# Optimization experiments

Measured on AMD Instinct MI355X. Metric: run time of the kernel, lower is better.

## Reference

```python
import jax, jax.numpy as jnp
import numpy as np

N = 100000
E = 3200000
D = 256
H = 8
DH = D // H
COEF = 1.0 / (DH ** 0.5)


def setup_inputs() -> dict:
    key = jax.random.key(0)
    ks = jax.random.split(key, 7)
    x = jax.random.normal(ks[0], (N, D), dtype=jnp.float32)
    W_qkv = jax.random.normal(ks[1], (D, 3 * D), dtype=jnp.float32) * (D ** -0.5)
    b_qkv = jax.random.normal(ks[2], (3 * D,), dtype=jnp.float32) * 0.01
    W_out = jax.random.normal(ks[3], (2 * D, D), dtype=jnp.float32) * ((2 * D) ** -0.5)
    b_out = jax.random.normal(ks[4], (D,), dtype=jnp.float32) * 0.01
    src = jax.random.randint(ks[5], (E,), 0, N, dtype=jnp.int64)
    dst = jax.random.randint(ks[6], (E,), 0, N, dtype=jnp.int64)
    return {"x": x, "W_qkv": W_qkv, "b_qkv": b_qkv, "W_out": W_out, "b_out": b_out, "src": src, "dst": dst}


def reference(x, W_qkv, b_qkv, W_out, b_out, src, dst):
    # qkv projection: [N, 3D] -> [N, H, 3*DH]
    qkv = (x @ W_qkv + b_qkv).reshape(N, H, 3 * DH)
    q, k, v = qkv[..., :DH], qkv[..., DH:2 * DH], qkv[..., 2 * DH:]
    # u_dot_v: per-edge dot(k[src], q[dst]) per head -> [E, H]
    scores = jnp.einsum('eh d, eh d -> eh'.replace(' ', ''), k[src], q[dst]) * COEF
    # edge_softmax over incoming edges of each destination node
    smax = jax.ops.segment_max(scores, dst, num_segments=N)          # [N, H]
    smax = jnp.where(jnp.isfinite(smax), smax, 0.0)                  # nodes w/o edges
    ex = jnp.exp(scores - smax[dst])                                 # [E, H]
    denom = jax.ops.segment_sum(ex, dst, num_segments=N)             # [N, H]
    probs = ex / jnp.maximum(denom[dst], 1e-20)                      # [E, H]
    # u_mul_e_sum: weighted aggregation of v[src] into dst -> [N, H, DH]
    message = jax.ops.segment_sum(v[src] * probs[:, :, None], dst, num_segments=N)
    message = message.reshape(N, D)
    out = jnp.concatenate([x, message], axis=1) @ W_out + b_out      # [N, D]
    return out
```

## Files before the change

### kernel.cpp

```cpp
#include <hip/hip_runtime.h>
#include <hip/hip_bf16.h>

typedef unsigned short u16;
typedef unsigned char u8;
typedef short bf16x8 __attribute__((ext_vector_type(8)));
typedef float f32x4 __attribute__((ext_vector_type(4)));
typedef float f32x2 __attribute__((ext_vector_type(2)));

#define NN 100000
#define EE 3200000
#define BUCKET 128
#define NCB 98
#define SUBCAP 4608

#define COARSE_BLOCKS 3125
#define CVT_BLOCKS 25000
#define TR1_BLOCKS 768
#define TR2_BLOCKS 512
#define PREP_BLOCKS (COARSE_BLOCKS + CVT_BLOCKS + TR1_BLOCKS + TR2_BLOCKS)
#define GEMM1_BLOCKS (782 * 6)

static constexpr float COEF = 0.17677669529663687f;

__device__ __forceinline__ u16 f2b(float f) {
    unsigned u = __float_as_uint(f);
    unsigned r = (u + 0x7fffu + ((u >> 16) & 1u)) >> 16;
    return (u16)r;
}

#define B2LO(w) __uint_as_float((w) << 16)
#define B2HI(w) __uint_as_float((w) & 0xffff0000u)

#define GLDS16(gp, lp) __builtin_amdgcn_global_load_lds( \
    (const __attribute__((address_space(1))) void*)(gp), \
    (__attribute__((address_space(3))) void*)(lp), 16, 0, 0)

__global__ __launch_bounds__(256) void prep_kernel(
    const float* __restrict__ x, u16* __restrict__ xb,
    const float* __restrict__ Wq, u16* __restrict__ WbT,
    const float* __restrict__ Wo, u16* __restrict__ WoT,
    const int* __restrict__ src, const int* __restrict__ dst,
    int* __restrict__ cur, uint2* __restrict__ ebuf) {
    __shared__ int lcnt[NCB];
    __shared__ int lbase[NCB];
    int b = blockIdx.x;
    int tid = threadIdx.x;
    if (b < COARSE_BLOCKS) {
        int e4 = b * 256 + tid;
        int xp = b & 7;
        int4 d = ((const int4*)dst)[e4];
        int4 s = ((const int4*)src)[e4];
        int cb0 = d.x >> 10, cb1 = d.y >> 10, cb2 = d.z >> 10, cb3 = d.w >> 10;
        if (tid < NCB) lcnt[tid] = 0;
        __syncthreads();
        int l0 = atomicAdd(&lcnt[cb0], 1);
        int l1 = atomicAdd(&lcnt[cb1], 1);
        int l2 = atomicAdd(&lcnt[cb2], 1);
        int l3 = atomicAdd(&lcnt[cb3], 1);
        __syncthreads();
        if (tid < NCB) {
            int c = lcnt[tid];
            lbase[tid] = c ? atomicAdd(&cur[(tid * 8 + xp) * 16], c) : 0;
        }
        __syncthreads();
        int p0 = lbase[cb0] + l0, p1 = lbase[cb1] + l1;
        int p2 = lbase[cb2] + l2, p3 = lbase[cb3] + l3;
        if (p0 < SUBCAP) ebuf[(size_t)(cb0 * 8 + xp) * SUBCAP + p0] = make_uint2((unsigned)s.x, (unsigned)d.x);
        if (p1 < SUBCAP) ebuf[(size_t)(cb1 * 8 + xp) * SUBCAP + p1] = make_uint2((unsigned)s.y, (unsigned)d.y);
        if (p2 < SUBCAP) ebuf[(size_t)(cb2 * 8 + xp) * SUBCAP + p2] = make_uint2((unsigned)s.z, (unsigned)d.z);
        if (p3 < SUBCAP) ebuf[(size_t)(cb3 * 8 + xp) * SUBCAP + p3] = make_uint2((unsigned)s.w, (unsigned)d.w);
        return;
    }
    b -= COARSE_BLOCKS;
    if (b < CVT_BLOCKS) {
        int i = b * 256 + tid;
        float4 v = ((const float4*)x)[i];
        ushort4 o;
        o.x = f2b(v.x); o.y = f2b(v.y); o.z = f2b(v.z); o.w = f2b(v.w);
        ((ushort4*)xb)[i] = o;
        return;
    }
    b -= CVT_BLOCKS;
    if (b < TR1_BLOCKS) {
        int idx = b * 256 + tid;
        int r = idx / 768, c = idx - r * 768;
        WbT[(size_t)c * 256 + r] = f2b(Wq[idx]);
        return;
    }
    b -= TR1_BLOCKS;
    {
        int idx = b * 256 + tid;
        int r = idx >> 8, c = idx & 255;
        WoT[(size_t)c * 512 + r] = f2b(Wo[idx]);
    }
}

__global__ __launch_bounds__(256) void attn_kernel(
    const u16* Q, const u8* __restrict__ KV8,
    const int* __restrict__ cnt, const int* __restrict__ esrc,
    u16* msg, int node0) {
    int node = node0 + blockIdx.x * 4 + (threadIdx.x >> 6);
    int lane = threadIdx.x & 63;
    int h = lane >> 3;
    int slot = lane & 7;
    int r0 = node * BUCKET;
    int r1 = r0 + min(cnt[node], BUCKET);

    f32x2 q2[16];
    {
        const uint4* qp = (const uint4*)(Q + (size_t)node * 256 + h * 32);
#pragma unroll
        for (int i = 0; i < 4; ++i) {
            uint4 wv = qp[i];
            q2[i * 4 + 0] = f32x2{B2LO(wv.x) * COEF, B2HI(wv.x) * COEF};
            q2[i * 4 + 1] = f32x2{B2LO(wv.y) * COEF, B2HI(wv.y) * COEF};
            q2[i * 4 + 2] = f32x2{B2LO(wv.z) * COEF, B2HI(wv.z) * COEF};
            q2[i * 4 + 3] = f32x2{B2LO(wv.w) * COEF, B2HI(wv.w) * COEF};
        }
    }

    float m = -3.0e38f, denom = 0.0f;
    f32x2 acc2[16];
#pragma unroll
    for (int i = 0; i < 16; ++i) acc2[i] = f32x2{0.0f, 0.0f};

#define DOTP(dd, u, j0) { f32x2 lo = __builtin_amdgcn_cvt_pk_f32_fp8(u, false); \
                          f32x2 hi = __builtin_amdgcn_cvt_pk_f32_fp8(u, true);  \
                          dd += q2[j0] * lo; dd += q2[(j0) + 1] * hi; }
#define ACCP(e2, u, j0) { f32x2 lo = __builtin_amdgcn_cvt_pk_f32_fp8(u, false); \
                          f32x2 hi = __builtin_amdgcn_cvt_pk_f32_fp8(u, true);  \
                          acc2[j0] += e2 * lo; acc2[(j0) + 1] += e2 * hi; }

    for (int base = r0; base < r1; base += 16) {
        int ja = base + slot, jb = base + 8 + slot;
        bool vA = ja < r1, vB = jb < r1;
        int sA = vA ? esrc[ja] : 0;
        int sB = vB ? esrc[jb] : 0;
        const uint4* pA = (const uint4*)(KV8 + (size_t)sA * 512 + h * 32);
        const uint4* pB = (const uint4*)(KV8 + (size_t)sB * 512 + h * 32);
        uint4 kA0 = pA[0], kA1 = pA[1], vA0 = pA[16], vA1 = pA[17];
        uint4 kB0 = pB[0], kB1 = pB[1], vB0 = pB[16], vB1 = pB[17];

        f32x2 dA2 = {0.0f, 0.0f}, dB2 = {0.0f, 0.0f};
        DOTP(dA2, kA0.x, 0);  DOTP(dA2, kA0.y, 2);  DOTP(dA2, kA0.z, 4);  DOTP(dA2, kA0.w, 6);
        DOTP(dA2, kA1.x, 8);  DOTP(dA2, kA1.y, 10); DOTP(dA2, kA1.z, 12); DOTP(dA2, kA1.w, 14);
        DOTP(dB2, kB0.x, 0);  DOTP(dB2, kB0.y, 2);  DOTP(dB2, kB0.z, 4);  DOTP(dB2, kB0.w, 6);
        DOTP(dB2, kB1.x, 8);  DOTP(dB2, kB1.y, 10); DOTP(dB2, kB1.z, 12); DOTP(dB2, kB1.w, 14);
        float dA = vA ? (dA2[0] + dA2[1]) : -3.0e38f;
        float dB = vB ? (dB2[0] + dB2[1]) : -3.0e38f;

        float dm = fmaxf(dA, dB);
        if (dm > m + 4.0f) {
            float scale = __expf(m - dm);
            m = dm;
            denom *= scale;
            f32x2 s2 = {scale, scale};
#pragma unroll
            for (int i = 0; i < 16; ++i) acc2[i] *= s2;
        }
        float exA = vA ? __expf(dA - m) : 0.0f;
        float exB = vB ? __expf(dB - m) : 0.0f;
        denom += exA + exB;
        f32x2 eA2 = {exA, exA}, eB2 = {exB, exB};
        ACCP(eA2, vA0.x, 0);  ACCP(eA2, vA0.y, 2);  ACCP(eA2, vA0.z, 4);  ACCP(eA2, vA0.w, 6);
        ACCP(eA2, vA1.x, 8);  ACCP(eA2, vA1.y, 10); ACCP(eA2, vA1.z, 12); ACCP(eA2, vA1.w, 14);
        ACCP(eB2, vB0.x, 0);  ACCP(eB2, vB0.y, 2);  ACCP(eB2, vB0.z, 4);  ACCP(eB2, vB0.w, 6);
        ACCP(eB2, vB1.x, 8);  ACCP(eB2, vB1.y, 10); ACCP(eB2, vB1.z, 12); ACCP(eB2, vB1.w, 14);
    }

    float mg = fmaxf(m, __shfl_xor(m, 1));
    mg = fmaxf(mg, __shfl_xor(mg, 2));
    mg = fmaxf(mg, __shfl_xor(mg, 4));
    float f = __expf(m - mg);
    float dn = denom * f;
    dn += __shfl_xor(dn, 1);
    dn += __shfl_xor(dn, 2);
    dn += __shfl_xor(dn, 4);
    float acc[32];
#pragma unroll
    for (int i = 0; i < 16; ++i) {
        acc[2 * i] = acc2[i][0] * f;
        acc[2 * i + 1] = acc2[i][1] * f;
    }

    float t16[16];
#pragma unroll
    for (int i = 0; i < 16; ++i) {
        float send = (slot & 1) ? acc[i] : acc[i + 16];
        float recv = __shfl_xor(send, 1);
        t16[i] = ((slot & 1) ? acc[i + 16] : acc[i]) + recv;
    }
    float t8[8];
#pragma unroll
    for (int i = 0; i < 8; ++i) {
        float send = (slot & 2) ? t16[i] : t16[i + 8];
        float recv = __shfl_xor(send, 2);
        t8[i] = ((slot & 2) ? t16[i + 8] : t16[i]) + recv;
    }
    float t4[4];
#pragma unroll
    for (int i = 0; i < 4; ++i) {
        float send = (slot & 4) ? t8[i] : t8[i + 4];
        float recv = __shfl_xor(send, 4);
        t4[i] = ((slot & 4) ? t8[i + 4] : t8[i]) + recv;
    }
    int dimbase = ((slot & 1) << 4) | ((slot & 2) << 2) | (slot & 4);

    float inv = 1.0f / fmaxf(dn, 1e-20f);
    ushort4 o;
    o.x = f2b(t4[0] * inv); o.y = f2b(t4[1] * inv);
    o.z = f2b(t4[2] * inv); o.w = f2b(t4[3] * inv);
    *(ushort4*)(msg + (size_t)node * 256 + h * 32 + dimbase) = o;
}

template <int MODE>
__global__ __launch_bounds__(256) void gemm_bt_kernel(
    const u16* __restrict__ A, const u16* __restrict__ A2, int splitK,
    const u16* __restrict__ Bt, const float* __restrict__ bias,
    int M, int Ntot, int Ktot, int ntiles_n, int nwg,
    float* __restrict__ outF, u16* __restrict__ outQ, u8* __restrict__ outKV,
    const uint2* __restrict__ ebuf, const int* __restrict__ cur,
    int* __restrict__ cnt, int* __restrict__ esrc, int fine_blocks) {
    __shared__ u16 As[128 * 64];
    __shared__ u16 Bs[128 * 64];
    if (MODE == 1 && (int)blockIdx.x < fine_blocks) {
        int cb = blockIdx.x;
        int nodebase = cb << 10;
        int* lcnt = (int*)As;
        for (int i = threadIdx.x; i < 1024; i += 256) lcnt[i] = 0;
        __syncthreads();
#pragma unroll 1
        for (int xp = 0; xp < 8; ++xp) {
            int sub = cb * 8 + xp;
            int n = cur[sub * 16];
            if (n > SUBCAP) n = SUBCAP;
            const uint2* base = ebuf + (size_t)sub * SUBCAP;
            for (int i = threadIdx.x; i < n; i += 256) {
                uint2 e = base[i];
                int dd = (int)e.y;
                int pos = atomicAdd(&lcnt[dd - nodebase], 1);
                if (pos < BUCKET) esrc[(size_t)dd * BUCKET + pos] = (int)e.x;
            }
        }
        __syncthreads();
        for (int i = threadIdx.x; i < 1024; i += 256) {
            int nd = nodebase + i;
            if (nd < NN) cnt[nd] = min(lcnt[i], BUCKET);
        }
        return;
    }
    const int bid = blockIdx.x - (MODE == 1 ? fine_blocks : 0);
    const int qq = nwg >> 3, rr = nwg & 7;
    const int xcd = bid & 7;
    const int tile = (xcd < rr ? xcd * (qq + 1) : rr * (qq + 1) + (xcd - rr) * qq) + (bid >> 3);
    const int tid = threadIdx.x;
    const int lane = tid & 63, wave = tid >> 6;
    const int wm = wave >> 1, wn = wave & 1;
    const int bm = tile / ntiles_n, bn = tile % ntiles_n;
    const int brow = bm * 128, bcol = bn * 128;

    f32x4 acc[4][4] = {};

    for (int k0 = 0; k0 < Ktot; k0 += 64) {
        const u16* Ab = (k0 < splitK) ? (A + k0) : (A2 + (k0 - splitK));
#pragma unroll
        for (int it = 0; it < 4; ++it) {
            int chunk = it * 256 + tid;
            int row = chunk >> 3;
            int cg = chunk & 7;
            int gcg = cg ^ (row & 7);
            int ga = brow + row; if (ga > M - 1) ga = M - 1;
            GLDS16(Ab + (size_t)ga * 256 + gcg * 8, As + (it * 256 + wave * 64) * 8);
            GLDS16(Bt + (size_t)(bcol + row) * Ktot + k0 + gcg * 8,
                   Bs + (it * 256 + wave * 64) * 8);
        }
        __syncthreads();
        const int kg = lane >> 4, rI = lane & 15, rx = lane & 7;
#pragma unroll
        for (int ks = 0; ks < 2; ++ks) {
            bf16x8 a[4], b[4];
#pragma unroll
            for (int m = 0; m < 4; ++m)
                a[m] = *(const bf16x8*)(As + (wm * 64 + m * 16 + rI) * 64 +
                                        (((ks * 4 + kg) ^ rx) * 8));
#pragma unroll
            for (int n = 0; n < 4; ++n)
                b[n] = *(const bf16x8*)(Bs + (wn * 64 + n * 16 + rI) * 64 +
                                        (((ks * 4 + kg) ^ rx) * 8));
#pragma unroll
            for (int m = 0; m < 4; ++m)
#pragma unroll
                for (int n = 0; n < 4; ++n)
                    acc[m][n] = __builtin_amdgcn_mfma_f32_16x16x32_bf16(a[m], b[n], acc[m][n], 0, 0, 0);
        }
        __syncthreads();
    }

#pragma unroll
    for (int m = 0; m < 4; ++m) {
        int growb = brow + wm * 64 + m * 16 + (lane >> 4) * 4;
#pragma unroll
        for (int n = 0; n < 4; ++n) {
            int gcol = bcol + wn * 64 + n * 16 + (lane & 15);
            float bi = bias[gcol];
#pragma unroll
            for (int r = 0; r < 4; ++r) {
                int grow = growb + r;
                if (grow >= M) continue;
                float c = acc[m][n][r] + bi;
                if (MODE == 0) {
                    outF[(size_t)grow * Ntot + gcol] = c;
                } else {
                    int hh = gcol / 96;
                    int rrm = gcol - hh * 96;
                    int sel = rrm >> 5;
                    int cc = hh * 32 + (rrm & 31);
                    if (sel == 0) {
                        outQ[(size_t)grow * 256 + cc] = f2b(c);
                    } else {
                        unsigned pv = __builtin_amdgcn_cvt_pk_fp8_f32(c, c, 0, false);
                        outKV[(size_t)grow * 512 + (sel - 1) * 256 + cc] = (u8)(pv & 0xff);
                    }
                }
            }
        }
    }
}

extern "C" void kernel_launch(void* const* d_in, const int* in_sizes, int n_in,
                              void* d_out, int out_size, void* d_ws, size_t ws_size,
                              hipStream_t stream) {
    const float* x = (const float*)d_in[0];
    const float* W_qkv = (const float*)d_in[1];
    const float* b_qkv = (const float*)d_in[2];
    const float* W_out = (const float*)d_in[3];
    const float* b_out = (const float*)d_in[4];
    const int* src = (const int*)d_in[5];
    const int* dst = (const int*)d_in[6];
    float* out = (float*)d_out;

    char* w = (char*)d_ws;
    size_t off = 0;
    auto alloc = [&](size_t bytes) -> char* {
        char* p = w + off;
        off += (bytes + 255) & ~(size_t)255;
        return p;
    };
    u16* xb = (u16*)alloc((size_t)NN * 256 * 2);
    u16* WbT = (u16*)alloc((size_t)768 * 256 * 2);
    u16* WoT = (u16*)alloc((size_t)256 * 512 * 2);
    u16* Qb = (u16*)alloc((size_t)NN * 256 * 2);
    u8* KV8 = (u8*)alloc((size_t)NN * 512);
    u16* msg = Qb;
    int* cnt = (int*)alloc((size_t)NN * 4);
    int* cur = (int*)alloc((size_t)NCB * 8 * 16 * 4);
    int* esrc = (int*)alloc((size_t)NN * BUCKET * 4);
    uint2* ebuf = (uint2*)alloc((size_t)NCB * 8 * SUBCAP * 8);

    hipMemsetAsync(cur, 0, (size_t)NCB * 8 * 16 * 4, stream);

    prep_kernel<<<PREP_BLOCKS, 256, 0, stream>>>(x, xb, W_qkv, WbT, W_out, WoT,
                                                 src, dst, cur, ebuf);

    gemm_bt_kernel<1><<<NCB + GEMM1_BLOCKS, 256, 0, stream>>>(
        xb, xb, 256, WbT, b_qkv, NN, 768, 256, 6, GEMM1_BLOCKS,
        nullptr, Qb, KV8, ebuf, cur, cnt, esrc, NCB);

    attn_kernel<<<NN / 8, 256, 0, stream>>>(Qb, KV8, cnt, esrc, msg, 0);
    attn_kernel<<<NN / 8, 256, 0, stream>>>(Qb, KV8, cnt, esrc, msg, NN / 2);

    gemm_bt_kernel<0><<<782 * 2, 256, 0, stream>>>(
        xb, msg, 256, WoT, b_out, NN, 256, 512, 2, 782 * 2,
        out, nullptr, nullptr, nullptr, nullptr, nullptr, nullptr, 0);
}
```

Before: 496.9 us.

## Overlap x-half of output GEMM with attention in one fused launch

The output projection is split along K into an x·W_out[:256] part and a msg·W_out[256:] part. The x part runs as extra blocks inside the attention launch, and the msg part runs afterwards in a separate kernel that adds into `out`. The two per-half attention launches become a single launch. The aim is to hide GEMM work behind the latency-bound attention gather and cut launch overhead. The cost is an extra read-modify-write of the full fp32 output. The clamp of cnt to BUCKET is also dropped.

```diff
diff --git a/kernel.cpp b/kernel.cpp
--- a/kernel.cpp
+++ b/kernel.cpp
@@ -19,6 +19,8 @@
 #define TR2_BLOCKS 512
 #define PREP_BLOCKS (COARSE_BLOCKS + CVT_BLOCKS + TR1_BLOCKS + TR2_BLOCKS)
 #define GEMM1_BLOCKS (782 * 6)
+#define G2A_BLOCKS (782 * 2)
+#define ATTN_BLOCKS (NN / 4)
 
 static constexpr float COEF = 0.17677669529663687f;
 
@@ -34,6 +36,93 @@
 #define GLDS16(gp, lp) __builtin_amdgcn_global_load_lds( \
     (const __attribute__((address_space(1))) void*)(gp), \
     (__attribute__((address_space(3))) void*)(lp), 16, 0, 0)
+
+template <int MODE>
+__device__ __forceinline__ void gemm_tile(
+    u16* As, u16* Bs,
+    const u16* __restrict__ A, const u16* __restrict__ A2, int splitK,
+    const u16* __restrict__ Bt, int ldb, const float* __restrict__ bias,
+    int M, int Ntot, int Ktot, int ntiles_n, int nwg, int bid,
+    float* outF, u16* outQ, u8* outKV) {
+    const int qq = nwg >> 3, rr2 = nwg & 7;
+    const int xcd = bid & 7;
+    const int tile = (xcd < rr2 ? xcd * (qq + 1) : rr2 * (qq + 1) + (xcd - rr2) * qq) + (bid >> 3);
+    const int tid = threadIdx.x;
+    const int lane = tid & 63, wave = tid >> 6;
+    const int wm = wave >> 1, wn = wave & 1;
+    const int bm = tile / ntiles_n, bn = tile % ntiles_n;
+    const int brow = bm * 128, bcol = bn * 128;
+
+    f32x4 acc[4][4] = {};
+
+    for (int k0 = 0; k0 < Ktot; k0 += 64) {
+        const u16* Ab = (k0 < splitK) ? (A + k0) : (A2 + (k0 - splitK));
+#pragma unroll
+        for (int it = 0; it < 4; ++it) {
+            int chunk = it * 256 + tid;
+            int row = chunk >> 3;
+            int cg = chunk & 7;
+            int gcg = cg ^ (row & 7);
+            int ga = brow + row; if (ga > M - 1) ga = M - 1;
+            GLDS16(Ab + (size_t)ga * 256 + gcg * 8, As + (it * 256 + wave * 64) * 8);
+            GLDS16(Bt + (size_t)(bcol + row) * ldb + k0 + gcg * 8,
+                   Bs + (it * 256 + wave * 64) * 8);
+        }
+        __syncthreads();
+        const int kg = lane >> 4, rI = lane & 15, rx = lane & 7;
+#pragma unroll
+        for (int ks = 0; ks < 2; ++ks) {
+            bf16x8 a[4], b[4];
+#pragma unroll
+            for (int m = 0; m < 4; ++m)
+                a[m] = *(const bf16x8*)(As + (wm * 64 + m * 16 + rI) * 64 +
+                                        (((ks * 4 + kg) ^ rx) * 8));
+#pragma unroll
+            for (int n = 0; n < 4; ++n)
+                b[n] = *(const bf16x8*)(Bs + (wn * 64 + n * 16 + rI) * 64 +
+                                        (((ks * 4 + kg) ^ rx) * 8));
+#pragma unroll
+            for (int m = 0; m < 4; ++m)
+#pragma unroll
+                for (int n = 0; n < 4; ++n)
+                    acc[m][n] = __builtin_amdgcn_mfma_f32_16x16x32_bf16(a[m], b[n], acc[m][n], 0, 0, 0);
+        }
+        __syncthreads();
+    }
+
+#pragma unroll
+    for (int m = 0; m < 4; ++m) {
+        int growb = brow + wm * 64 + m * 16 + (lane >> 4) * 4;
+#pragma unroll
+        for (int n = 0; n < 4; ++n) {
+            int gcol = bcol + wn * 64 + n * 16 + (lane & 15);
+            float bi = (MODE == 2) ? 0.0f : bias[gcol];
+#pragma unroll
+            for (int r = 0; r < 4; ++r) {
+                int grow = growb + r;
+                if (grow >= M) continue;
+                float c = acc[m][n][r] + bi;
+                if (MODE == 0) {
+                    outF[(size_t)grow * Ntot + gcol] = c;
+                } else if (MODE == 2) {
+                    size_t oi = (size_t)grow * Ntot + gcol;
+                    outF[oi] = c + outF[oi];
+                } else {
+                    int hh = gcol / 96;
+                    int rrm = gcol - hh * 96;
+                    int sel = rrm >> 5;
+                    int cc = hh * 32 + (rrm & 31);
+                    if (sel == 0) {
+                        outQ[(size_t)grow * 256 + cc] = f2b(c);
+                    } else {
+                        unsigned pv = __builtin_amdgcn_cvt_pk_fp8_f32(c, c, 0, false);
+                        outKV[(size_t)grow * 512 + (sel - 1) * 256 + cc] = (u8)(pv & 0xff);
+                    }
+                }
+            }
+        }
+    }
+}
 
 __global__ __launch_bounds__(256) void prep_kernel(
     const float* __restrict__ x, u16* __restrict__ xb,
@@ -95,135 +184,14 @@
     }
 }
 
-__global__ __launch_bounds__(256) void attn_kernel(
-    const u16* Q, const u8* __restrict__ KV8,
-    const int* __restrict__ cnt, const int* __restrict__ esrc,
-    u16* msg, int node0) {
-    int node = node0 + blockIdx.x * 4 + (threadIdx.x >> 6);
-    int lane = threadIdx.x & 63;
-    int h = lane >> 3;
-    int slot = lane & 7;
-    int r0 = node * BUCKET;
-    int r1 = r0 + min(cnt[node], BUCKET);
-
-    f32x2 q2[16];
-    {
-        const uint4* qp = (const uint4*)(Q + (size_t)node * 256 + h * 32);
-#pragma unroll
-        for (int i = 0; i < 4; ++i) {
-            uint4 wv = qp[i];
-            q2[i * 4 + 0] = f32x2{B2LO(wv.x) * COEF, B2HI(wv.x) * COEF};
-            q2[i * 4 + 1] = f32x2{B2LO(wv.y) * COEF, B2HI(wv.y) * COEF};
-            q2[i * 4 + 2] = f32x2{B2LO(wv.z) * COEF, B2HI(wv.z) * COEF};
-            q2[i * 4 + 3] = f32x2{B2LO(wv.w) * COEF, B2HI(wv.w) * COEF};
-        }
-    }
-
-    float m = -3.0e38f, denom = 0.0f;
-    f32x2 acc2[16];
-#pragma unroll
-    for (int i = 0; i < 16; ++i) acc2[i] = f32x2{0.0f, 0.0f};
-
-#define DOTP(dd, u, j0) { f32x2 lo = __builtin_amdgcn_cvt_pk_f32_fp8(u, false); \
-                          f32x2 hi = __builtin_amdgcn_cvt_pk_f32_fp8(u, true);  \
-                          dd += q2[j0] * lo; dd += q2[(j0) + 1] * hi; }
-#define ACCP(e2, u, j0) { f32x2 lo = __builtin_amdgcn_cvt_pk_f32_fp8(u, false); \
-                          f32x2 hi = __builtin_amdgcn_cvt_pk_f32_fp8(u, true);  \
-                          acc2[j0] += e2 * lo; acc2[(j0) + 1] += e2 * hi; }
-
-    for (int base = r0; base < r1; base += 16) {
-        int ja = base + slot, jb = base + 8 + slot;
-        bool vA = ja < r1, vB = jb < r1;
-        int sA = vA ? esrc[ja] : 0;
-        int sB = vB ? esrc[jb] : 0;
-        const uint4* pA = (const uint4*)(KV8 + (size_t)sA * 512 + h * 32);
-        const uint4* pB = (const uint4*)(KV8 + (size_t)sB * 512 + h * 32);
-        uint4 kA0 = pA[0], kA1 = pA[1], vA0 = pA[16], vA1 = pA[17];
-        uint4 kB0 = pB[0], kB1 = pB[1], vB0 = pB[16], vB1 = pB[17];
-
-        f32x2 dA2 = {0.0f, 0.0f}, dB2 = {0.0f, 0.0f};
-        DOTP(dA2, kA0.x, 0);  DOTP(dA2, kA0.y, 2);  DOTP(dA2, kA0.z, 4);  DOTP(dA2, kA0.w, 6);
-        DOTP(dA2, kA1.x, 8);  DOTP(dA2, kA1.y, 10); DOTP(dA2, kA1.z, 12); DOTP(dA2, kA1.w, 14);
-        DOTP(dB2, kB0.x, 0);  DOTP(dB2, kB0.y, 2);  DOTP(dB2, kB0.z, 4);  DOTP(dB2, kB0.w, 6);
-        DOTP(dB2, kB1.x, 8);  DOTP(dB2, kB1.y, 10); DOTP(dB2, kB1.z, 12); DOTP(dB2, kB1.w, 14);
-        float dA = vA ? (dA2[0] + dA2[1]) : -3.0e38f;
-        float dB = vB ? (dB2[0] + dB2[1]) : -3.0e38f;
-
-        float dm = fmaxf(dA, dB);
-        if (dm > m + 4.0f) {
-            float scale = __expf(m - dm);
-            m = dm;
-            denom *= scale;
-            f32x2 s2 = {scale, scale};
-#pragma unroll
-            for (int i = 0; i < 16; ++i) acc2[i] *= s2;
-        }
-        float exA = vA ? __expf(dA - m) : 0.0f;
-        float exB = vB ? __expf(dB - m) : 0.0f;
-        denom += exA + exB;
-        f32x2 eA2 = {exA, exA}, eB2 = {exB, exB};
-        ACCP(eA2, vA0.x, 0);  ACCP(eA2, vA0.y, 2);  ACCP(eA2, vA0.z, 4);  ACCP(eA2, vA0.w, 6);
-        ACCP(eA2, vA1.x, 8);  ACCP(eA2, vA1.y, 10); ACCP(eA2, vA1.z, 12); ACCP(eA2, vA1.w, 14);
-        ACCP(eB2, vB0.x, 0);  ACCP(eB2, vB0.y, 2);  ACCP(eB2, vB0.z, 4);  ACCP(eB2, vB0.w, 6);
-        ACCP(eB2, vB1.x, 8);  ACCP(eB2, vB1.y, 10); ACCP(eB2, vB1.z, 12); ACCP(eB2, vB1.w, 14);
-    }
-
-    float mg = fmaxf(m, __shfl_xor(m, 1));
-    mg = fmaxf(mg, __shfl_xor(mg, 2));
-    mg = fmaxf(mg, __shfl_xor(mg, 4));
-    float f = __expf(m - mg);
-    float dn = denom * f;
-    dn += __shfl_xor(dn, 1);
-    dn += __shfl_xor(dn, 2);
-    dn += __shfl_xor(dn, 4);
-    float acc[32];
-#pragma unroll
-    for (int i = 0; i < 16; ++i) {
-        acc[2 * i] = acc2[i][0] * f;
-        acc[2 * i + 1] = acc2[i][1] * f;
-    }
-
-    float t16[16];
-#pragma unroll
-    for (int i = 0; i < 16; ++i) {
-        float send = (slot & 1) ? acc[i] : acc[i + 16];
-        float recv = __shfl_xor(send, 1);
-        t16[i] = ((slot & 1) ? acc[i + 16] : acc[i]) + recv;
-    }
-    float t8[8];
-#pragma unroll
-    for (int i = 0; i < 8; ++i) {
-        float send = (slot & 2) ? t16[i] : t16[i + 8];
-        float recv = __shfl_xor(send, 2);
-        t8[i] = ((slot & 2) ? t16[i + 8] : t16[i]) + recv;
-    }
-    float t4[4];
-#pragma unroll
-    for (int i = 0; i < 4; ++i) {
-        float send = (slot & 4) ? t8[i] : t8[i + 4];
-        float recv = __shfl_xor(send, 4);
-        t4[i] = ((slot & 4) ? t8[i + 4] : t8[i]) + recv;
-    }
-    int dimbase = ((slot & 1) << 4) | ((slot & 2) << 2) | (slot & 4);
-
-    float inv = 1.0f / fmaxf(dn, 1e-20f);
-    ushort4 o;
-    o.x = f2b(t4[0] * inv); o.y = f2b(t4[1] * inv);
-    o.z = f2b(t4[2] * inv); o.w = f2b(t4[3] * inv);
-    *(ushort4*)(msg + (size_t)node * 256 + h * 32 + dimbase) = o;
-}
-
-template <int MODE>
-__global__ __launch_bounds__(256) void gemm_bt_kernel(
-    const u16* __restrict__ A, const u16* __restrict__ A2, int splitK,
-    const u16* __restrict__ Bt, const float* __restrict__ bias,
-    int M, int Ntot, int Ktot, int ntiles_n, int nwg,
-    float* __restrict__ outF, u16* __restrict__ outQ, u8* __restrict__ outKV,
+__global__ __launch_bounds__(256) void qkv_kernel(
+    const u16* __restrict__ A, const u16* __restrict__ Bt, const float* __restrict__ bias,
+    u16* __restrict__ outQ, u8* __restrict__ outKV,
     const uint2* __restrict__ ebuf, const int* __restrict__ cur,
-    int* __restrict__ cnt, int* __restrict__ esrc, int fine_blocks) {
+    int* __restrict__ cnt, int* __restrict__ esrc) {
     __shared__ u16 As[128 * 64];
     __shared__ u16 Bs[128 * 64];
-    if (MODE == 1 && (int)blockIdx.x < fine_blocks) {
+    if ((int)blockIdx.x < NCB) {
         int cb = blockIdx.x;
         int nodebase = cb << 10;
         int* lcnt = (int*)As;
@@ -249,82 +217,143 @@
         }
         return;
     }
-    const int bid = blockIdx.x - (MODE == 1 ? fine_blocks : 0);
-    const int qq = nwg >> 3, rr = nwg & 7;
-    const int xcd = bid & 7;
-    const int tile = (xcd < rr ? xcd * (qq + 1) : rr * (qq + 1) + (xcd - rr) * qq) + (bid >> 3);
-    const int tid = threadIdx.x;
-    const int lane = tid & 63, wave = tid >> 6;
-    const int wm = wave >> 1, wn = wave & 1;
-    const int bm = tile / ntiles_n, bn = tile % ntiles_n;
-    const int brow = bm * 128, bcol = bn * 128;
-
-    f32x4 acc[4][4] = {};
-
-    for (int k0 = 0; k0 < Ktot; k0 += 64) {
-        const u16* Ab = (k0 < splitK) ? (A + k0) : (A2 + (k0 - splitK));
-#pragma unroll
-        for (int it = 0; it < 4; ++it) {
-            int chunk = it * 256 + tid;
-            int row = chunk >> 3;
-            int cg = chunk & 7;
-            int gcg = cg ^ (row & 7);
-            int ga = brow + row; if (ga > M - 1) ga = M - 1;
-            GLDS16(Ab + (size_t)ga * 256 + gcg * 8, As + (it * 256 + wave * 64) * 8);
-            GLDS16(Bt + (size_t)(bcol + row) * Ktot + k0 + gcg * 8,
-                   Bs + (it * 256 + wave * 64) * 8);
-        }
-        __syncthreads();
-        const int kg = lane >> 4, rI = lane & 15, rx = lane & 7;
-#pragma unroll
-        for (int ks = 0; ks < 2; ++ks) {
-            bf16x8 a[4], b[4];
-#pragma unroll
-            for (int m = 0; m < 4; ++m)
-                a[m] = *(const bf16x8*)(As + (wm * 64 + m * 16 + rI) * 64 +
-                                        (((ks * 4 + kg) ^ rx) * 8));
-#pragma unroll
-            for (int n = 0; n < 4; ++n)
-                b[n] = *(const bf16x8*)(Bs + (wn * 64 + n * 16 + rI) * 64 +
-                                        (((ks * 4 + kg) ^ rx) * 8));
-#pragma unroll
-            for (int m = 0; m < 4; ++m)
-#pragma unroll
-                for (int n = 0; n < 4; ++n)
-                    acc[m][n] = __builtin_amdgcn_mfma_f32_16x16x32_bf16(a[m], b[n], acc[m][n], 0, 0, 0);
-        }
-        __syncthreads();
-    }
-
-#pragma unroll
-    for (int m = 0; m < 4; ++m) {
-        int growb = brow + wm * 64 + m * 16 + (lane >> 4) * 4;
-#pragma unroll
-        for (int n = 0; n < 4; ++n) {
-            int gcol = bcol + wn * 64 + n * 16 + (lane & 15);
-            float bi = bias[gcol];
-#pragma unroll
-            for (int r = 0; r < 4; ++r) {
-                int grow = growb + r;
-                if (grow >= M) continue;
-                float c = acc[m][n][r] + bi;
-                if (MODE == 0) {
-                    outF[(size_t)grow * Ntot + gcol] = c;
-                } else {
-                    int hh = gcol / 96;
-                    int rrm = gcol - hh * 96;
-                    int sel = rrm >> 5;
-                    int cc = hh * 32 + (rrm & 31);
-                    if (sel == 0) {
-                        outQ[(size_t)grow * 256 + cc] = f2b(c);
-                    } else {
-                        unsigned pv = __builtin_amdgcn_cvt_pk_fp8_f32(c, c, 0, false);
-                        outKV[(size_t)grow * 512 + (sel - 1) * 256 + cc] = (u8)(pv & 0xff);
-                    }
-                }
-            }
-        }
-    }
+    gemm_tile<1>(As, Bs, A, A, 256, Bt, 256, bias, NN, 768, 256, 6, GEMM1_BLOCKS,
+                 (int)blockIdx.x - NCB, nullptr, outQ, outKV);
+}
+
+__global__ __launch_bounds__(256) void attn_gemm_kernel(
+    const u16* Q, const u8* __restrict__ KV8,
+    const int* __restrict__ cnt, const int* __restrict__ esrc, u16* msg,
+    const u16* __restrict__ xb, const u16* __restrict__ WoT,
+    const float* __restrict__ b_out, float* __restrict__ out) {
+    __shared__ u16 As[128 * 64];
+    __shared__ u16 Bs[128 * 64];
+    if ((int)blockIdx.x < G2A_BLOCKS) {
+        gemm_tile<0>(As, Bs, xb, xb, 256, WoT, 512, b_out, NN, 256, 256, 2, G2A_BLOCKS,
+                     (int)blockIdx.x, out, nullptr, nullptr);
+        return;
+    }
+    int node = ((int)blockIdx.x - G2A_BLOCKS) * 4 + (threadIdx.x >> 6);
+    int lane = threadIdx.x & 63;
+    int h = lane >> 3;
+    int slot = lane & 7;
+    int r0 = node * BUCKET;
+    int r1 = r0 + cnt[node];
+
+    f32x2 q2[16];
+    {
+        const uint4* qp = (const uint4*)(Q + (size_t)node * 256 + h * 32);
+#pragma unroll
+        for (int i = 0; i < 4; ++i) {
+            uint4 wv = qp[i];
+            q2[i * 4 + 0] = f32x2{B2LO(wv.x) * COEF, B2HI(wv.x) * COEF};
+            q2[i * 4 + 1] = f32x2{B2LO(wv.y) * COEF, B2HI(wv.y) * COEF};
+            q2[i * 4 + 2] = f32x2{B2LO(wv.z) * COEF, B2HI(wv.z) * COEF};
+            q2[i * 4 + 3] = f32x2{B2LO(wv.w) * COEF, B2HI(wv.w) * COEF};
+        }
+    }
+
+    float m = -3.0e38f, denom = 0.0f;
+    f32x2 acc2[16];
+#pragma unroll
+    for (int i = 0; i < 16; ++i) acc2[i] = f32x2{0.0f, 0.0f};
+
+#define DOTP(dd, u, j0) { f32x2 lo = __builtin_amdgcn_cvt_pk_f32_fp8(u, false); \
+                          f32x2 hi = __builtin_amdgcn_cvt_pk_f32_fp8(u, true);  \
+                          dd += q2[j0] * lo; dd += q2[(j0) + 1] * hi; }
+#define ACCP(e2, u, j0) { f32x2 lo = __builtin_amdgcn_cvt_pk_f32_fp8(u, false); \
+                          f32x2 hi = __builtin_amdgcn_cvt_pk_f32_fp8(u, true);  \
+                          acc2[j0] += e2 * lo; acc2[(j0) + 1] += e2 * hi; }
+
+    for (int base = r0; base < r1; base += 16) {
+        int ja = base + slot, jb = base + 8 + slot;
+        bool vA = ja < r1, vB = jb < r1;
+        int sA = vA ? esrc[ja] : 0;
+        int sB = vB ? esrc[jb] : 0;
+        const uint4* pA = (const uint4*)(KV8 + (size_t)sA * 512 + h * 32);
+        const uint4* pB = (const uint4*)(KV8 + (size_t)sB * 512 + h * 32);
+        uint4 kA0 = pA[0], kA1 = pA[1], vA0 = pA[16], vA1 = pA[17];
+        uint4 kB0 = pB[0], kB1 = pB[1], vB0 = pB[16], vB1 = pB[17];
+
+        f32x2 dA2 = {0.0f, 0.0f}, dB2 = {0.0f, 0.0f};
+        DOTP(dA2, kA0.x, 0);  DOTP(dA2, kA0.y, 2);  DOTP(dA2, kA0.z, 4);  DOTP(dA2, kA0.w, 6);
+        DOTP(dA2, kA1.x, 8);  DOTP(dA2, kA1.y, 10); DOTP(dA2, kA1.z, 12); DOTP(dA2, kA1.w, 14);
+        DOTP(dB2, kB0.x, 0);  DOTP(dB2, kB0.y, 2);  DOTP(dB2, kB0.z, 4);  DOTP(dB2, kB0.w, 6);
+        DOTP(dB2, kB1.x, 8);  DOTP(dB2, kB1.y, 10); DOTP(dB2, kB1.z, 12); DOTP(dB2, kB1.w, 14);
+        float dA = vA ? (dA2[0] + dA2[1]) : -3.0e38f;
+        float dB = vB ? (dB2[0] + dB2[1]) : -3.0e38f;
+
+        float dm = fmaxf(dA, dB);
+        if (dm > m + 4.0f) {
+            float scale = __expf(m - dm);
+            m = dm;
+            denom *= scale;
+            f32x2 s2 = {scale, scale};
+#pragma unroll
+            for (int i = 0; i < 16; ++i) acc2[i] *= s2;
+        }
+        float exA = vA ? __expf(dA - m) : 0.0f;
+        float exB = vB ? __expf(dB - m) : 0.0f;
+        denom += exA + exB;
+        f32x2 eA2 = {exA, exA}, eB2 = {exB, exB};
+        ACCP(eA2, vA0.x, 0);  ACCP(eA2, vA0.y, 2);  ACCP(eA2, vA0.z, 4);  ACCP(eA2, vA0.w, 6);
+        ACCP(eA2, vA1.x, 8);  ACCP(eA2, vA1.y, 10); ACCP(eA2, vA1.z, 12); ACCP(eA2, vA1.w, 14);
+        ACCP(eB2, vB0.x, 0);  ACCP(eB2, vB0.y, 2);  ACCP(eB2, vB0.z, 4);  ACCP(eB2, vB0.w, 6);
+        ACCP(eB2, vB1.x, 8);  ACCP(eB2, vB1.y, 10); ACCP(eB2, vB1.z, 12); ACCP(eB2, vB1.w, 14);
+    }
+
+    float mg = fmaxf(m, __shfl_xor(m, 1));
+    mg = fmaxf(mg, __shfl_xor(mg, 2));
+    mg = fmaxf(mg, __shfl_xor(mg, 4));
+    float f = __expf(m - mg);
+    float dn = denom * f;
+    dn += __shfl_xor(dn, 1);
+    dn += __shfl_xor(dn, 2);
+    dn += __shfl_xor(dn, 4);
+    float acc[32];
+#pragma unroll
+    for (int i = 0; i < 16; ++i) {
+        acc[2 * i] = acc2[i][0] * f;
+        acc[2 * i + 1] = acc2[i][1] * f;
+    }
+
+    float t16[16];
+#pragma unroll
+    for (int i = 0; i < 16; ++i) {
+        float send = (slot & 1) ? acc[i] : acc[i + 16];
+        float recv = __shfl_xor(send, 1);
+        t16[i] = ((slot & 1) ? acc[i + 16] : acc[i]) + recv;
+    }
+    float t8[8];
+#pragma unroll
+    for (int i = 0; i < 8; ++i) {
+        float send = (slot & 2) ? t16[i] : t16[i + 8];
+        float recv = __shfl_xor(send, 2);
+        t8[i] = ((slot & 2) ? t16[i + 8] : t16[i]) + recv;
+    }
+    float t4[4];
+#pragma unroll
+    for (int i = 0; i < 4; ++i) {
+        float send = (slot & 4) ? t8[i] : t8[i + 4];
+        float recv = __shfl_xor(send, 4);
+        t4[i] = ((slot & 4) ? t8[i + 4] : t8[i]) + recv;
+    }
+    int dimbase = ((slot & 1) << 4) | ((slot & 2) << 2) | (slot & 4);
+
+    float inv = 1.0f / fmaxf(dn, 1e-20f);
+    ushort4 o;
+    o.x = f2b(t4[0] * inv); o.y = f2b(t4[1] * inv);
+    o.z = f2b(t4[2] * inv); o.w = f2b(t4[3] * inv);
+    *(ushort4*)(msg + (size_t)node * 256 + h * 32 + dimbase) = o;
+}
+
+__global__ __launch_bounds__(256) void out_kernel(
+    const u16* __restrict__ msg, const u16* __restrict__ WoT,
+    float* __restrict__ out) {
+    __shared__ u16 As[128 * 64];
+    __shared__ u16 Bs[128 * 64];
+    gemm_tile<2>(As, Bs, msg, msg, 256, WoT + 256, 512, nullptr, NN, 256, 256, 2,
+                 G2A_BLOCKS, (int)blockIdx.x, out, nullptr, nullptr);
 }
 
 extern "C" void kernel_launch(void* const* d_in, const int* in_sizes, int n_in,
@@ -362,14 +391,11 @@
     prep_kernel<<<PREP_BLOCKS, 256, 0, stream>>>(x, xb, W_qkv, WbT, W_out, WoT,
                                                  src, dst, cur, ebuf);
 
-    gemm_bt_kernel<1><<<NCB + GEMM1_BLOCKS, 256, 0, stream>>>(
-        xb, xb, 256, WbT, b_qkv, NN, 768, 256, 6, GEMM1_BLOCKS,
-        nullptr, Qb, KV8, ebuf, cur, cnt, esrc, NCB);
-
-    attn_kernel<<<NN / 8, 256, 0, stream>>>(Qb, KV8, cnt, esrc, msg, 0);
-    attn_kernel<<<NN / 8, 256, 0, stream>>>(Qb, KV8, cnt, esrc, msg, NN / 2);
-
-    gemm_bt_kernel<0><<<782 * 2, 256, 0, stream>>>(
-        xb, msg, 256, WoT, b_out, NN, 256, 512, 2, 782 * 2,
-        out, nullptr, nullptr, nullptr, nullptr, nullptr, nullptr, 0);
-}
+    qkv_kernel<<<NCB + GEMM1_BLOCKS, 256, 0, stream>>>(xb, WbT, b_qkv, Qb, KV8,
+                                                       ebuf, cur, cnt, esrc);
+
+    attn_gemm_kernel<<<G2A_BLOCKS + ATTN_BLOCKS, 256, 0, stream>>>(
+        Qb, KV8, cnt, esrc, msg, xb, WoT, b_out, out);
+
+    out_kernel<<<G2A_BLOCKS, 256, 0, stream>>>(msg, WoT, out);
+}
```

Result: slower. 708.3 us (+42.5%).
